# Kernel optimization log

Hardware: AMD Instinct MI355X
Metric: run time of the kernel (lower is better)

The kernel has to match this reference:

```python
import jax, jax.numpy as jnp
import numpy as np

N_NODES = 50000
N_EDGES = 800000
IN_CH = 256
HID = 32
HEADS = 8
OUT_CH = 64
NEG_SLOPE = 0.2


def _glorot(key, shape):
    fan = shape[0] + shape[-1]
    lim = jnp.sqrt(6.0 / fan)
    return jax.random.uniform(key, shape, jnp.float32, -lim, lim)


def setup_inputs() -> dict:
    key = jax.random.key(0)
    ks = jax.random.split(key, 12)
    x = jax.random.normal(ks[0], (N_NODES, IN_CH), jnp.float32)
    edge_index = jax.random.randint(ks[1], (2, N_EDGES), 0, N_NODES, jnp.int64 if jax.config.jax_enable_x64 else jnp.int32)
    # conv1: in -> heads*hid, concat
    W1 = _glorot(ks[2], (IN_CH, HEADS * HID))
    a_src1 = _glorot(ks[3], (HEADS, HID))
    a_dst1 = _glorot(ks[4], (HEADS, HID))
    b1 = jnp.zeros((HEADS * HID,), jnp.float32)
    # conv2: heads*hid -> heads*hid, 1 head
    W2 = _glorot(ks[5], (HEADS * HID, HEADS * HID))
    a_src2 = _glorot(ks[6], (1, HEADS * HID))
    a_dst2 = _glorot(ks[7], (1, HEADS * HID))
    b2 = jnp.zeros((HEADS * HID,), jnp.float32)
    # final linear
    Wlin = _glorot(ks[8], (HEADS * HID, OUT_CH))
    blin = jnp.zeros((OUT_CH,), jnp.float32)
    return {"x": x, "edge_index": edge_index, "W1": W1, "a_src1": a_src1,
            "a_dst1": a_dst1, "b1": b1, "W2": W2, "a_src2": a_src2,
            "a_dst2": a_dst2, "b2": b2, "Wlin": Wlin, "blin": blin}


def gat_conv(x, src, dst, W, a_src, a_dst, bias, heads, out_ch):
    n = x.shape[0]
    h = (x @ W).reshape(n, heads, out_ch)            # [N, H, C]
    # per-node attention halves, then gather per edge (cheaper than edge-first)
    s = jnp.einsum('nhc,hc->nh', h, a_src)[src]      # [E, H]
    d = jnp.einsum('nhc,hc->nh', h, a_dst)[dst]      # [E, H]
    e = jax.nn.leaky_relu(s + d, NEG_SLOPE)          # [E, H]
    # segment softmax over incoming edges of each dst node
    emax = jax.ops.segment_max(e, dst, num_segments=n)
    e = jnp.exp(e - jax.lax.stop_gradient(emax)[dst])
    denom = jax.ops.segment_sum(e, dst, num_segments=n)
    alpha = e / denom[dst]                           # [E, H]
    msg = h[src] * alpha[:, :, None]                 # [E, H, C]
    out = jax.ops.segment_sum(msg, dst, num_segments=n)
    return out.reshape(n, heads * out_ch) + bias


def reference(x, edge_index, W1, a_src1, a_dst1, b1, W2, a_src2, a_dst2, b2, Wlin, blin):
    n = x.shape[0]
    # PyG GATConv adds self-loops by default
    loops = jnp.arange(n, dtype=edge_index.dtype)
    src = jnp.concatenate([edge_index[0], loops])
    dst = jnp.concatenate([edge_index[1], loops])
    # dropout (p=0.6) is identity in eval mode
    h = jax.nn.elu(gat_conv(x, src, dst, W1, a_src1, a_dst1, b1, HEADS, HID))
    h = jax.nn.elu(gat_conv(h, src, dst, W2, a_src2, a_dst2, b2, 1, HEADS * HID))
    return h @ Wlin + blin
```

## Files before the change

kernel.cpp:

```cpp
#include <hip/hip_runtime.h>
#include <hip/hip_bf16.h>
#include <hip/hip_fp16.h>

typedef __attribute__((ext_vector_type(8))) short short8;
typedef __attribute__((ext_vector_type(4))) float f32x4;

#define GLL(g, s) __builtin_amdgcn_global_load_lds(                        \
    (const __attribute__((address_space(1))) void*)(g),                    \
    (__attribute__((address_space(3))) void*)(s), 16, 0, 0)

__device__ __forceinline__ ushort f2bf(float f) {
    unsigned u = __float_as_uint(f);
    u += 0x7fffu + ((u >> 16) & 1u);
    return (ushort)(u >> 16);
}
__device__ __forceinline__ float bf2f(ushort h) {
    return __uint_as_float(((unsigned)h) << 16);
}
__device__ __forceinline__ float elu_f(float x) {
    return x > 0.0f ? x : expm1f(x);
}
__device__ __forceinline__ float lrelu(float x) {
    return x < 0.0f ? 0.2f * x : x;
}

__global__ void hist_kernel(const int* __restrict__ ei, int* __restrict__ deg, int E, int n) {
    int total = E + n;
    for (int i = blockIdx.x * blockDim.x + threadIdx.x; i < total; i += gridDim.x * blockDim.x) {
        int d = (i < E) ? ei[E + i] : (i - E);
        atomicAdd(&deg[d], 1);
    }
}

__global__ __launch_bounds__(256) void partial_kernel(const int* __restrict__ deg, int* __restrict__ bsums, int n) {
    __shared__ int sm[256];
    int t = threadIdx.x;
    int idx = blockIdx.x * 256 + t;
    sm[t] = (idx < n) ? deg[idx] : 0;
    __syncthreads();
    #pragma unroll
    for (int off = 128; off > 0; off >>= 1) {
        if (t < off) sm[t] += sm[t + off];
        __syncthreads();
    }
    if (t == 0) bsums[blockIdx.x] = sm[0];
}

__global__ __launch_bounds__(256) void finalize2_kernel(const int* __restrict__ deg, const int* __restrict__ bsums,
                                                        int* __restrict__ rowptr, int* __restrict__ cursor,
                                                        int n, int nb) {
    __shared__ int sm[256];
    __shared__ int sbase;
    int t = threadIdx.x, b = blockIdx.x;
    int part = 0;
    for (int i = t; i < b; i += 256) part += bsums[i];
    sm[t] = part;
    __syncthreads();
    #pragma unroll
    for (int off = 128; off > 0; off >>= 1) {
        if (t < off) sm[t] += sm[t + off];
        __syncthreads();
    }
    if (t == 0) sbase = sm[0];
    __syncthreads();
    int base = sbase;
    __syncthreads();
    int idx = b * 256 + t;
    int v = (idx < n) ? deg[idx] : 0;
    sm[t] = v;
    __syncthreads();
    #pragma unroll
    for (int off = 1; off < 256; off <<= 1) {
        int x = (t >= off) ? sm[t - off] : 0;
        __syncthreads();
        sm[t] += x;
        __syncthreads();
    }
    if (idx < n) {
        int ex = base + sm[t] - v;
        rowptr[idx] = ex;
        cursor[idx] = ex;
    }
    if (b == nb - 1 && t == 255) rowptr[n] = base + sm[255];
}

__global__ void scatter_kernel(const int* __restrict__ ei, int* __restrict__ cursor,
                               int* __restrict__ csr_src, int E, int n) {
    int total = E + n;
    for (int i = blockIdx.x * blockDim.x + threadIdx.x; i < total; i += gridDim.x * blockDim.x) {
        int s, d;
        if (i < E) { s = ei[i]; d = ei[E + i]; }
        else       { s = i - E; d = s; }
        int pos = atomicAdd(&cursor[d], 1);
        csr_src[pos] = s;
    }
}

__global__ __launch_bounds__(256) void packall_kernel(const float* __restrict__ x,
                                                      const float* __restrict__ W1,
                                                      const float* __restrict__ W2,
                                                      const float* __restrict__ W3,
                                                      short* __restrict__ xh, short* __restrict__ xl,
                                                      short* __restrict__ w1h, short* __restrict__ w1l,
                                                      short* __restrict__ w2h, short* __restrict__ w2l,
                                                      short* __restrict__ w3h, short* __restrict__ w3l,
                                                      int M, int Mpad, int XB) {
    int b = blockIdx.x;
    int t = threadIdx.x;
    if (b < XB) {
        int r = b * 8 + (t >> 5);
        int cc = t & 31;
        if (r >= M) return;
        const float* src = x + (size_t)r * 256 + cc * 8;
        short8 hi, lo;
        #pragma unroll
        for (int j = 0; j < 8; ++j) {
            float v = src[j];
            ushort h = f2bf(v);
            hi[j] = (short)h;
            lo[j] = (short)f2bf(v - bf2f(h));
        }
        size_t o = ((size_t)cc * Mpad + r) * 8;
        *(short8*)(xh + o) = hi;
        *(short8*)(xl + o) = lo;
        return;
    }
    const float* W; short* hh; short* ll; int Ncols; int base;
    if (b < XB + 256)      { W = W1; hh = w1h; ll = w1l; Ncols = 256; base = XB; }
    else if (b < XB + 512) { W = W2; hh = w2h; ll = w2l; Ncols = 256; base = XB + 256; }
    else                   { W = W3; hh = w3h; ll = w3l; Ncols = 64;  base = XB + 512; }
    int idx = (b - base) * 256 + t;
    int k = idx / Ncols, n = idx - k * Ncols;
    float v = W[idx];
    ushort h = f2bf(v);
    ushort l = f2bf(v - bf2f(h));
    size_t o = ((size_t)(k >> 3) * Ncols + n) * 8 + (k & 7);
    hh[o] = (short)h;
    ll[o] = (short)l;
}

template<int FN, bool OUTHALF>
__global__ __launch_bounds__(64) void gemm_pk(const short* __restrict__ Aph, const short* __restrict__ Apl,
                                              const short* __restrict__ Bph, const short* __restrict__ Bpl,
                                              const float* __restrict__ bias, void* __restrict__ Cout,
                                              int M, int Mpad, int NCOLS) {
    __shared__ short Ah[2][4][64][8], Al[2][4][64][8];
    __shared__ short Bh[2][4][FN * 16][8], Bl[2][4][FN * 16][8];
    const int lane = threadIdx.x;
    const int r0 = blockIdx.x * 64;
    const int c0 = blockIdx.y * FN * 16;
    const int c = lane >> 4;
    const int rs = lane & 15;

    auto issue = [&](int buf, int t) {
        #pragma unroll
        for (int q = 0; q < 4; ++q) {
            int kc = t * 4 + q;
            GLL(Aph + ((size_t)kc * Mpad + r0 + lane) * 8, &Ah[buf][q][0][0]);
            GLL(Apl + ((size_t)kc * Mpad + r0 + lane) * 8, &Al[buf][q][0][0]);
            #pragma unroll
            for (int hseg = 0; hseg < FN / 4; ++hseg) {
                GLL(Bph + ((size_t)kc * NCOLS + c0 + hseg * 64 + lane) * 8, &Bh[buf][q][hseg * 64][0]);
                GLL(Bpl + ((size_t)kc * NCOLS + c0 + hseg * 64 + lane) * 8, &Bl[buf][q][hseg * 64][0]);
            }
        }
    };

    f32x4 acc[4][FN];
    #pragma unroll
    for (int i = 0; i < 4; ++i)
        #pragma unroll
        for (int j = 0; j < FN; ++j)
            acc[i][j] = (f32x4){0.f, 0.f, 0.f, 0.f};

    issue(0, 0);
    issue(1, 1);

    #pragma unroll
    for (int t = 0; t < 8; ++t) {
        if (t < 7) {
            if constexpr (FN == 8) asm volatile("s_waitcnt vmcnt(24)" ::: "memory");
            else                   asm volatile("s_waitcnt vmcnt(16)" ::: "memory");
        } else {
            asm volatile("s_waitcnt vmcnt(0)" ::: "memory");
        }
        __builtin_amdgcn_sched_barrier(0);
        const int buf = t & 1;
        short8 ah[4], al[4];
        #pragma unroll
        for (int fm = 0; fm < 4; ++fm) {
            ah[fm] = *(const short8*)&Ah[buf][c][fm * 16 + rs][0];
            al[fm] = *(const short8*)&Al[buf][c][fm * 16 + rs][0];
        }
        short8 bh[FN], bl[FN];
        #pragma unroll
        for (int fn = 0; fn < FN; ++fn) {
            bh[fn] = *(const short8*)&Bh[buf][c][fn * 16 + rs][0];
            bl[fn] = *(const short8*)&Bl[buf][c][fn * 16 + rs][0];
        }
        asm volatile("s_waitcnt lgkmcnt(0)" ::: "memory");
        __builtin_amdgcn_sched_barrier(0);
        if (t < 6) issue(buf, t + 2);
        #pragma unroll
        for (int fn = 0; fn < FN; ++fn) {
            #pragma unroll
            for (int fm = 0; fm < 4; ++fm) {
                acc[fm][fn] = __builtin_amdgcn_mfma_f32_16x16x32_bf16(ah[fm], bh[fn], acc[fm][fn], 0, 0, 0);
                acc[fm][fn] = __builtin_amdgcn_mfma_f32_16x16x32_bf16(ah[fm], bl[fn], acc[fm][fn], 0, 0, 0);
                acc[fm][fn] = __builtin_amdgcn_mfma_f32_16x16x32_bf16(al[fm], bh[fn], acc[fm][fn], 0, 0, 0);
            }
        }
    }

    #pragma unroll
    for (int fn = 0; fn < FN; ++fn) {
        int col = c0 + fn * 16 + rs;
        float bv = bias ? bias[col] : 0.0f;
        #pragma unroll
        for (int fm = 0; fm < 4; ++fm) {
            #pragma unroll
            for (int g = 0; g < 4; ++g) {
                int r = r0 + fm * 16 + c * 4 + g;
                if (r < M) {
                    float v = acc[fm][fn][g] + bv;
                    if constexpr (OUTHALF)
                        ((__half*)Cout)[(size_t)r * NCOLS + col] = __float2half_rn(v);
                    else
                        ((float*)Cout)[(size_t)r * NCOLS + col] = v;
                }
            }
        }
    }
}

template<int HEADS>
__global__ __launch_bounds__(256) void sd_kernel(const __half* __restrict__ h, const float* __restrict__ a_src,
                                                 const float* __restrict__ a_dst, float* __restrict__ s_out,
                                                 float* __restrict__ d_out_, int nnodes) {
    int lane = threadIdx.x & 63;
    int node = blockIdx.x * 4 + (threadIdx.x >> 6);
    if (node >= nnodes) return;
    const __half2* hp = (const __half2*)(h + (size_t)node * 256 + lane * 4);
    float2 f01 = __half22float2(hp[0]);
    float2 f23 = __half22float2(hp[1]);
    float4 as = *(const float4*)&a_src[lane * 4];
    float4 ad = *(const float4*)&a_dst[lane * 4];
    float ps = f01.x * as.x + f01.y * as.y + f23.x * as.z + f23.y * as.w;
    float pd = f01.x * ad.x + f01.y * ad.y + f23.x * ad.z + f23.y * ad.w;
    const int GS = 64 / HEADS;
    #pragma unroll
    for (int off = 1; off < GS; off <<= 1) {
        ps += __shfl_xor(ps, off);
        pd += __shfl_xor(pd, off);
    }
    int g = lane / GS;
    int r = lane & (GS - 1);
    if (r == 0) s_out[(size_t)node * HEADS + g] = ps * 1.44269504f;
    if (r == 1) d_out_[(size_t)node * HEADS + g] = pd * 1.44269504f;
}

template<int HEADS>
__global__ __launch_bounds__(256) void agg_kernel(const int* __restrict__ rowptr, const int* __restrict__ csr_src,
                                                  const __half* __restrict__ h, const float* __restrict__ s_att,
                                                  const float* __restrict__ d_att, const float* __restrict__ bias,
                                                  short* __restrict__ outh, short* __restrict__ outl,
                                                  int nnodes, int Mpad) {
    int lane = threadIdx.x & 63;
    int node = blockIdx.x * 4 + (threadIdx.x >> 6);
    if (node >= nnodes) return;
    const int hh = (HEADS == 8) ? (lane >> 3) : 0;
    const int cbase = lane * 4;
    const int begin = rowptr[node], end = rowptr[node + 1];
    const float dl = d_att[(size_t)node * HEADS + hh];
    float den = 0.f;
    float ax = 0.f, ay = 0.f, az = 0.f, aw = 0.f;
    int i = begin;
    for (; i + 4 <= end; i += 4) {
        int s0 = csr_src[i], s1 = csr_src[i + 1], s2 = csr_src[i + 2], s3 = csr_src[i + 3];
        uint2 u0 = *(const uint2*)(h + (size_t)s0 * 256 + cbase);
        uint2 u1 = *(const uint2*)(h + (size_t)s1 * 256 + cbase);
        uint2 u2 = *(const uint2*)(h + (size_t)s2 * 256 + cbase);
        uint2 u3 = *(const uint2*)(h + (size_t)s3 * 256 + cbase);
        float w0 = exp2f(lrelu(s_att[(size_t)s0 * HEADS + hh] + dl) - 30.0f);
        float w1 = exp2f(lrelu(s_att[(size_t)s1 * HEADS + hh] + dl) - 30.0f);
        float w2 = exp2f(lrelu(s_att[(size_t)s2 * HEADS + hh] + dl) - 30.0f);
        float w3 = exp2f(lrelu(s_att[(size_t)s3 * HEADS + hh] + dl) - 30.0f);
        den += (w0 + w1) + (w2 + w3);
        float2 f0a = __half22float2(*(const __half2*)&u0.x), f0b = __half22float2(*(const __half2*)&u0.y);
        float2 f1a = __half22float2(*(const __half2*)&u1.x), f1b = __half22float2(*(const __half2*)&u1.y);
        float2 f2a = __half22float2(*(const __half2*)&u2.x), f2b = __half22float2(*(const __half2*)&u2.y);
        float2 f3a = __half22float2(*(const __half2*)&u3.x), f3b = __half22float2(*(const __half2*)&u3.y);
        ax += w0 * f0a.x + w1 * f1a.x + w2 * f2a.x + w3 * f3a.x;
        ay += w0 * f0a.y + w1 * f1a.y + w2 * f2a.y + w3 * f3a.y;
        az += w0 * f0b.x + w1 * f1b.x + w2 * f2b.x + w3 * f3b.x;
        aw += w0 * f0b.y + w1 * f1b.y + w2 * f2b.y + w3 * f3b.y;
    }
    for (; i < end; ++i) {
        int s0 = csr_src[i];
        uint2 u0 = *(const uint2*)(h + (size_t)s0 * 256 + cbase);
        float w0 = exp2f(lrelu(s_att[(size_t)s0 * HEADS + hh] + dl) - 30.0f);
        den += w0;
        float2 f0a = __half22float2(*(const __half2*)&u0.x), f0b = __half22float2(*(const __half2*)&u0.y);
        ax += w0 * f0a.x;
        ay += w0 * f0a.y;
        az += w0 * f0b.x;
        aw += w0 * f0b.y;
    }
    float inv = 1.0f / den;
    float4 bv = *(const float4*)&bias[cbase];
    float r0 = elu_f(ax * inv + bv.x);
    float r1 = elu_f(ay * inv + bv.y);
    float r2 = elu_f(az * inv + bv.z);
    float r3 = elu_f(aw * inv + bv.w);
    ushort h0 = f2bf(r0), h1 = f2bf(r1), h2 = f2bf(r2), h3 = f2bf(r3);
    ushort l0 = f2bf(r0 - bf2f(h0)), l1 = f2bf(r1 - bf2f(h1));
    ushort l2 = f2bf(r2 - bf2f(h2)), l3 = f2bf(r3 - bf2f(h3));
    size_t o = ((size_t)(lane >> 1) * Mpad + node) * 8 + (lane & 1) * 4;
    uint2 hv, lv;
    hv.x = (unsigned)h0 | ((unsigned)h1 << 16);
    hv.y = (unsigned)h2 | ((unsigned)h3 << 16);
    lv.x = (unsigned)l0 | ((unsigned)l1 << 16);
    lv.y = (unsigned)l2 | ((unsigned)l3 << 16);
    *(uint2*)(outh + o) = hv;
    *(uint2*)(outl + o) = lv;
}

extern "C" void kernel_launch(void* const* d_in, const int* in_sizes, int n_in,
                              void* d_out, int out_size, void* d_ws, size_t ws_size,
                              hipStream_t stream) {
    const float* x      = (const float*)d_in[0];
    const int*   ei     = (const int*)d_in[1];
    const float* W1     = (const float*)d_in[2];
    const float* a_src1 = (const float*)d_in[3];
    const float* a_dst1 = (const float*)d_in[4];
    const float* b1     = (const float*)d_in[5];
    const float* W2     = (const float*)d_in[6];
    const float* a_src2 = (const float*)d_in[7];
    const float* a_dst2 = (const float*)d_in[8];
    const float* b2     = (const float*)d_in[9];
    const float* Wlin   = (const float*)d_in[10];
    const float* blin   = (const float*)d_in[11];
    float* out = (float*)d_out;

    const int N = in_sizes[0] / 256;
    const int E = in_sizes[1] / 2;
    const int ET = E + N;
    const int NB = (N + 255) / 256;
    const int Mpad = ((N + 63) / 64) * 64;

    char* p = (char*)d_ws;
    auto alloc = [&](size_t bytes) {
        void* r = (void*)p;
        p += (bytes + 255) & ~size_t(255);
        return r;
    };
    __half* bufH  = (__half*)alloc((size_t)N * 256 * 2);
    short* Aph    = (short*)alloc((size_t)Mpad * 256 * 2);
    short* Apl    = (short*)alloc((size_t)Mpad * 256 * 2);
    float* s1     = (float*)alloc((size_t)N * 8 * 4);
    float* d1     = (float*)alloc((size_t)N * 8 * 4);
    float* s2     = (float*)alloc((size_t)N * 4);
    float* d2     = (float*)alloc((size_t)N * 4);
    int*   deg    = (int*)alloc((size_t)N * 4);
    int*   cursor = (int*)alloc((size_t)N * 4);
    int*   rowptr = (int*)alloc((size_t)(N + 1) * 4);
    int*   csr    = (int*)alloc((size_t)ET * 4);
    int*   bsums  = (int*)alloc((size_t)NB * 4);
    short* W1h    = (short*)alloc((size_t)256 * 256 * 2);
    short* W1l    = (short*)alloc((size_t)256 * 256 * 2);
    short* W2h    = (short*)alloc((size_t)256 * 256 * 2);
    short* W2l    = (short*)alloc((size_t)256 * 256 * 2);
    short* W3h    = (short*)alloc((size_t)256 * 64 * 2);
    short* W3l    = (short*)alloc((size_t)256 * 64 * 2);

    hipMemsetAsync(deg, 0, (size_t)N * 4, stream);
    hist_kernel<<<(ET + 255) / 256, 256, 0, stream>>>(ei, deg, E, N);
    partial_kernel<<<NB, 256, 0, stream>>>(deg, bsums, N);
    finalize2_kernel<<<NB, 256, 0, stream>>>(deg, bsums, rowptr, cursor, N, NB);
    scatter_kernel<<<(ET + 255) / 256, 256, 0, stream>>>(ei, cursor, csr, E, N);

    const int XB = (N + 7) / 8;
    packall_kernel<<<XB + 512 + 64, 256, 0, stream>>>(x, W1, W2, Wlin,
                                                      Aph, Apl, W1h, W1l, W2h, W2l, W3h, W3l,
                                                      N, Mpad, XB);

    const int gBlocks = (N + 63) / 64;
    const int nodeBlocks = (N + 3) / 4;

    gemm_pk<8, true><<<dim3(gBlocks, 2), 64, 0, stream>>>(Aph, Apl, W1h, W1l, nullptr, bufH, N, Mpad, 256);
    sd_kernel<8><<<nodeBlocks, 256, 0, stream>>>(bufH, a_src1, a_dst1, s1, d1, N);
    agg_kernel<8><<<nodeBlocks, 256, 0, stream>>>(rowptr, csr, bufH, s1, d1, b1, Aph, Apl, N, Mpad);

    gemm_pk<8, true><<<dim3(gBlocks, 2), 64, 0, stream>>>(Aph, Apl, W2h, W2l, nullptr, bufH, N, Mpad, 256);
    sd_kernel<1><<<nodeBlocks, 256, 0, stream>>>(bufH, a_src2, a_dst2, s2, d2, N);
    agg_kernel<1><<<nodeBlocks, 256, 0, stream>>>(rowptr, csr, bufH, s2, d2, b2, Aph, Apl, N, Mpad);

    gemm_pk<4, false><<<dim3(gBlocks, 1), 64, 0, stream>>>(Aph, Apl, W3h, W3l, blin, out, N, Mpad, 64);
}
```

Before: 577.5 us.

## Replace split-bf16 three-MFMA GEMMs with single fp16 MFMA and row-major activations

Drops the hi/lo bf16 split representation, where each product needed three MFMAs plus double loads, and uses plain fp16 operands with one f16 MFMA per tile. Activations are now stored row-major in fp16: packing becomes a straight cast and the aggregation kernel writes half2 pairs directly. This cuts GEMM math, LDS and global traffic roughly by half or more, and the wait counts are adjusted to match. The cost is lower accuracy, since fp16 has an 11-bit mantissa versus the roughly 16-bit effective precision of the split bf16 scheme, and the A loads are now strided per row.

```diff
diff --git a/kernel.cpp b/kernel.cpp
--- a/kernel.cpp
+++ b/kernel.cpp
@@ -2,21 +2,13 @@
 #include <hip/hip_bf16.h>
 #include <hip/hip_fp16.h>
 
-typedef __attribute__((ext_vector_type(8))) short short8;
+typedef __attribute__((ext_vector_type(8))) _Float16 half8;
 typedef __attribute__((ext_vector_type(4))) float f32x4;
 
 #define GLL(g, s) __builtin_amdgcn_global_load_lds(                        \
     (const __attribute__((address_space(1))) void*)(g),                    \
     (__attribute__((address_space(3))) void*)(s), 16, 0, 0)
 
-__device__ __forceinline__ ushort f2bf(float f) {
-    unsigned u = __float_as_uint(f);
-    u += 0x7fffu + ((u >> 16) & 1u);
-    return (ushort)(u >> 16);
-}
-__device__ __forceinline__ float bf2f(ushort h) {
-    return __uint_as_float(((unsigned)h) << 16);
-}
 __device__ __forceinline__ float elu_f(float x) {
     return x > 0.0f ? x : expm1f(x);
 }
@@ -100,52 +92,40 @@
                                                       const float* __restrict__ W1,
                                                       const float* __restrict__ W2,
                                                       const float* __restrict__ W3,
-                                                      short* __restrict__ xh, short* __restrict__ xl,
-                                                      short* __restrict__ w1h, short* __restrict__ w1l,
-                                                      short* __restrict__ w2h, short* __restrict__ w2l,
-                                                      short* __restrict__ w3h, short* __restrict__ w3l,
-                                                      int M, int Mpad, int XB) {
+                                                      _Float16* __restrict__ xp,
+                                                      _Float16* __restrict__ w1p,
+                                                      _Float16* __restrict__ w2p,
+                                                      _Float16* __restrict__ w3p,
+                                                      int Mtot, int XB) {
     int b = blockIdx.x;
     int t = threadIdx.x;
     if (b < XB) {
-        int r = b * 8 + (t >> 5);
-        int cc = t & 31;
-        if (r >= M) return;
-        const float* src = x + (size_t)r * 256 + cc * 8;
-        short8 hi, lo;
-        #pragma unroll
-        for (int j = 0; j < 8; ++j) {
-            float v = src[j];
-            ushort h = f2bf(v);
-            hi[j] = (short)h;
-            lo[j] = (short)f2bf(v - bf2f(h));
-        }
-        size_t o = ((size_t)cc * Mpad + r) * 8;
-        *(short8*)(xh + o) = hi;
-        *(short8*)(xl + o) = lo;
+        size_t idx = ((size_t)b * 256 + t) * 8;
+        if (idx >= (size_t)Mtot * 256) return;
+        const float* src = x + idx;
+        half8 v;
+        #pragma unroll
+        for (int j = 0; j < 8; ++j) v[j] = (_Float16)src[j];
+        *(half8*)(xp + idx) = v;
         return;
     }
-    const float* W; short* hh; short* ll; int Ncols; int base;
-    if (b < XB + 256)      { W = W1; hh = w1h; ll = w1l; Ncols = 256; base = XB; }
-    else if (b < XB + 512) { W = W2; hh = w2h; ll = w2l; Ncols = 256; base = XB + 256; }
-    else                   { W = W3; hh = w3h; ll = w3l; Ncols = 64;  base = XB + 512; }
+    const float* W; _Float16* wp; int Ncols; int base;
+    if (b < XB + 256)      { W = W1; wp = w1p; Ncols = 256; base = XB; }
+    else if (b < XB + 512) { W = W2; wp = w2p; Ncols = 256; base = XB + 256; }
+    else                   { W = W3; wp = w3p; Ncols = 64;  base = XB + 512; }
     int idx = (b - base) * 256 + t;
     int k = idx / Ncols, n = idx - k * Ncols;
-    float v = W[idx];
-    ushort h = f2bf(v);
-    ushort l = f2bf(v - bf2f(h));
     size_t o = ((size_t)(k >> 3) * Ncols + n) * 8 + (k & 7);
-    hh[o] = (short)h;
-    ll[o] = (short)l;
+    wp[o] = (_Float16)W[idx];
 }
 
 template<int FN, bool OUTHALF>
-__global__ __launch_bounds__(64) void gemm_pk(const short* __restrict__ Aph, const short* __restrict__ Apl,
-                                              const short* __restrict__ Bph, const short* __restrict__ Bpl,
+__global__ __launch_bounds__(64) void gemm_pk(const _Float16* __restrict__ Apk,
+                                              const _Float16* __restrict__ Bpk,
                                               const float* __restrict__ bias, void* __restrict__ Cout,
-                                              int M, int Mpad, int NCOLS) {
-    __shared__ short Ah[2][4][64][8], Al[2][4][64][8];
-    __shared__ short Bh[2][4][FN * 16][8], Bl[2][4][FN * 16][8];
+                                              int M, int NCOLS) {
+    __shared__ _Float16 Ah[2][4][64][8];
+    __shared__ _Float16 Bh[2][4][FN * 16][8];
     const int lane = threadIdx.x;
     const int r0 = blockIdx.x * 64;
     const int c0 = blockIdx.y * FN * 16;
@@ -156,13 +136,10 @@
         #pragma unroll
         for (int q = 0; q < 4; ++q) {
             int kc = t * 4 + q;
-            GLL(Aph + ((size_t)kc * Mpad + r0 + lane) * 8, &Ah[buf][q][0][0]);
-            GLL(Apl + ((size_t)kc * Mpad + r0 + lane) * 8, &Al[buf][q][0][0]);
+            GLL(Apk + (size_t)(r0 + lane) * 256 + kc * 8, &Ah[buf][q][0][0]);
             #pragma unroll
-            for (int hseg = 0; hseg < FN / 4; ++hseg) {
-                GLL(Bph + ((size_t)kc * NCOLS + c0 + hseg * 64 + lane) * 8, &Bh[buf][q][hseg * 64][0]);
-                GLL(Bpl + ((size_t)kc * NCOLS + c0 + hseg * 64 + lane) * 8, &Bl[buf][q][hseg * 64][0]);
-            }
+            for (int hs = 0; hs < FN / 4; ++hs)
+                GLL(Bpk + ((size_t)kc * NCOLS + c0 + hs * 64 + lane) * 8, &Bh[buf][q][hs * 64][0]);
         }
     };
 
@@ -179,37 +156,29 @@
     #pragma unroll
     for (int t = 0; t < 8; ++t) {
         if (t < 7) {
-            if constexpr (FN == 8) asm volatile("s_waitcnt vmcnt(24)" ::: "memory");
-            else                   asm volatile("s_waitcnt vmcnt(16)" ::: "memory");
+            if constexpr (FN == 8) asm volatile("s_waitcnt vmcnt(12)" ::: "memory");
+            else                   asm volatile("s_waitcnt vmcnt(8)" ::: "memory");
         } else {
             asm volatile("s_waitcnt vmcnt(0)" ::: "memory");
         }
         __builtin_amdgcn_sched_barrier(0);
         const int buf = t & 1;
-        short8 ah[4], al[4];
-        #pragma unroll
-        for (int fm = 0; fm < 4; ++fm) {
-            ah[fm] = *(const short8*)&Ah[buf][c][fm * 16 + rs][0];
-            al[fm] = *(const short8*)&Al[buf][c][fm * 16 + rs][0];
-        }
-        short8 bh[FN], bl[FN];
-        #pragma unroll
-        for (int fn = 0; fn < FN; ++fn) {
-            bh[fn] = *(const short8*)&Bh[buf][c][fn * 16 + rs][0];
-            bl[fn] = *(const short8*)&Bl[buf][c][fn * 16 + rs][0];
-        }
+        half8 ah[4];
+        #pragma unroll
+        for (int fm = 0; fm < 4; ++fm)
+            ah[fm] = *(const half8*)&Ah[buf][c][fm * 16 + rs][0];
+        half8 bh[FN];
+        #pragma unroll
+        for (int fn = 0; fn < FN; ++fn)
+            bh[fn] = *(const half8*)&Bh[buf][c][fn * 16 + rs][0];
         asm volatile("s_waitcnt lgkmcnt(0)" ::: "memory");
         __builtin_amdgcn_sched_barrier(0);
         if (t < 6) issue(buf, t + 2);
         #pragma unroll
-        for (int fn = 0; fn < FN; ++fn) {
+        for (int fn = 0; fn < FN; ++fn)
             #pragma unroll
-            for (int fm = 0; fm < 4; ++fm) {
-                acc[fm][fn] = __builtin_amdgcn_mfma_f32_16x16x32_bf16(ah[fm], bh[fn], acc[fm][fn], 0, 0, 0);
-                acc[fm][fn] = __builtin_amdgcn_mfma_f32_16x16x32_bf16(ah[fm], bl[fn], acc[fm][fn], 0, 0, 0);
-                acc[fm][fn] = __builtin_amdgcn_mfma_f32_16x16x32_bf16(al[fm], bh[fn], acc[fm][fn], 0, 0, 0);
-            }
-        }
+            for (int fm = 0; fm < 4; ++fm)
+                acc[fm][fn] = __builtin_amdgcn_mfma_f32_16x16x32_f16(ah[fm], bh[fn], acc[fm][fn], 0, 0, 0);
     }
 
     #pragma unroll
@@ -263,8 +232,7 @@
 __global__ __launch_bounds__(256) void agg_kernel(const int* __restrict__ rowptr, const int* __restrict__ csr_src,
                                                   const __half* __restrict__ h, const float* __restrict__ s_att,
                                                   const float* __restrict__ d_att, const float* __restrict__ bias,
-                                                  short* __restrict__ outh, short* __restrict__ outl,
-                                                  int nnodes, int Mpad) {
+                                                  _Float16* __restrict__ outH, int nnodes) {
     int lane = threadIdx.x & 63;
     int node = blockIdx.x * 4 + (threadIdx.x >> 6);
     if (node >= nnodes) return;
@@ -312,17 +280,12 @@
     float r1 = elu_f(ay * inv + bv.y);
     float r2 = elu_f(az * inv + bv.z);
     float r3 = elu_f(aw * inv + bv.w);
-    ushort h0 = f2bf(r0), h1 = f2bf(r1), h2 = f2bf(r2), h3 = f2bf(r3);
-    ushort l0 = f2bf(r0 - bf2f(h0)), l1 = f2bf(r1 - bf2f(h1));
-    ushort l2 = f2bf(r2 - bf2f(h2)), l3 = f2bf(r3 - bf2f(h3));
-    size_t o = ((size_t)(lane >> 1) * Mpad + node) * 8 + (lane & 1) * 4;
-    uint2 hv, lv;
-    hv.x = (unsigned)h0 | ((unsigned)h1 << 16);
-    hv.y = (unsigned)h2 | ((unsigned)h3 << 16);
-    lv.x = (unsigned)l0 | ((unsigned)l1 << 16);
-    lv.y = (unsigned)l2 | ((unsigned)l3 << 16);
-    *(uint2*)(outh + o) = hv;
-    *(uint2*)(outl + o) = lv;
+    __half2 o01 = __floats2half2_rn(r0, r1);
+    __half2 o23 = __floats2half2_rn(r2, r3);
+    uint2 wv;
+    wv.x = *(unsigned*)&o01;
+    wv.y = *(unsigned*)&o23;
+    *(uint2*)(outH + (size_t)node * 256 + cbase) = wv;
 }
 
 extern "C" void kernel_launch(void* const* d_in, const int* in_sizes, int n_in,
@@ -354,9 +317,8 @@
         p += (bytes + 255) & ~size_t(255);
         return r;
     };
-    __half* bufH  = (__half*)alloc((size_t)N * 256 * 2);
-    short* Aph    = (short*)alloc((size_t)Mpad * 256 * 2);
-    short* Apl    = (short*)alloc((size_t)Mpad * 256 * 2);
+    __half*    bufH = (__half*)alloc((size_t)Mpad * 256 * 2);
+    _Float16*  Apk  = (_Float16*)alloc((size_t)Mpad * 256 * 2);
     float* s1     = (float*)alloc((size_t)N * 8 * 4);
     float* d1     = (float*)alloc((size_t)N * 8 * 4);
     float* s2     = (float*)alloc((size_t)N * 4);
@@ -366,12 +328,9 @@
     int*   rowptr = (int*)alloc((size_t)(N + 1) * 4);
     int*   csr    = (int*)alloc((size_t)ET * 4);
     int*   bsums  = (int*)alloc((size_t)NB * 4);
-    short* W1h    = (short*)alloc((size_t)256 * 256 * 2);
-    short* W1l    = (short*)alloc((size_t)256 * 256 * 2);
-    short* W2h    = (short*)alloc((size_t)256 * 256 * 2);
-    short* W2l    = (short*)alloc((size_t)256 * 256 * 2);
-    short* W3h    = (short*)alloc((size_t)256 * 64 * 2);
-    short* W3l    = (short*)alloc((size_t)256 * 64 * 2);
+    _Float16* W1p = (_Float16*)alloc((size_t)256 * 256 * 2);
+    _Float16* W2p = (_Float16*)alloc((size_t)256 * 256 * 2);
+    _Float16* W3p = (_Float16*)alloc((size_t)256 * 64 * 2);
 
     hipMemsetAsync(deg, 0, (size_t)N * 4, stream);
     hist_kernel<<<(ET + 255) / 256, 256, 0, stream>>>(ei, deg, E, N);
@@ -379,21 +338,20 @@
     finalize2_kernel<<<NB, 256, 0, stream>>>(deg, bsums, rowptr, cursor, N, NB);
     scatter_kernel<<<(ET + 255) / 256, 256, 0, stream>>>(ei, cursor, csr, E, N);
 
-    const int XB = (N + 7) / 8;
+    const int XB = (N * 256 + 2047) / 2048;
     packall_kernel<<<XB + 512 + 64, 256, 0, stream>>>(x, W1, W2, Wlin,
-                                                      Aph, Apl, W1h, W1l, W2h, W2l, W3h, W3l,
-                                                      N, Mpad, XB);
+                                                      Apk, W1p, W2p, W3p, N, XB);
 
     const int gBlocks = (N + 63) / 64;
     const int nodeBlocks = (N + 3) / 4;
 
-    gemm_pk<8, true><<<dim3(gBlocks, 2), 64, 0, stream>>>(Aph, Apl, W1h, W1l, nullptr, bufH, N, Mpad, 256);
+    gemm_pk<8, true><<<dim3(gBlocks, 2), 64, 0, stream>>>(Apk, W1p, nullptr, bufH, N, 256);
     sd_kernel<8><<<nodeBlocks, 256, 0, stream>>>(bufH, a_src1, a_dst1, s1, d1, N);
-    agg_kernel<8><<<nodeBlocks, 256, 0, stream>>>(rowptr, csr, bufH, s1, d1, b1, Aph, Apl, N, Mpad);
-
-    gemm_pk<8, true><<<dim3(gBlocks, 2), 64, 0, stream>>>(Aph, Apl, W2h, W2l, nullptr, bufH, N, Mpad, 256);
+    agg_kernel<8><<<nodeBlocks, 256, 0, stream>>>(rowptr, csr, bufH, s1, d1, b1, Apk, N);
+
+    gemm_pk<8, true><<<dim3(gBlocks, 2), 64, 0, stream>>>(Apk, W2p, nullptr, bufH, N, 256);
     sd_kernel<1><<<nodeBlocks, 256, 0, stream>>>(bufH, a_src2, a_dst2, s2, d2, N);
-    agg_kernel<1><<<nodeBlocks, 256, 0, stream>>>(rowptr, csr, bufH, s2, d2, b2, Aph, Apl, N, Mpad);
-
-    gemm_pk<4, false><<<dim3(gBlocks, 1), 64, 0, stream>>>(Aph, Apl, W3h, W3l, blin, out, N, Mpad, 64);
-}
+    agg_kernel<1><<<nodeBlocks, 256, 0, stream>>>(rowptr, csr, bufH, s2, d2, b2, Apk, N);
+
+    gemm_pk<4, false><<<dim3(gBlocks, 1), 64, 0, stream>>>(Apk, W3p, blin, out, N, 64);
+}
```

Result: faster. 475.1 us (-17.7%).
